# Performance work log

Hardware: AMD Instinct MI355X
Metric: run time of the kernel (lower is better)

Reference implementation:

```python
import jax, jax.numpy as jnp
import numpy as np

# physical params matching init_kwargs: (eta, gamma, Lambda, omega, n), dt
ETA, GAMMA, LAMBDA, OMEGA, NBAR = 0.8, 0.3, 0.5, 1.0, 2.0
DT = 1e-3


def _consts():
    a_diag = jnp.diag(jnp.full((2,), -0.5 * GAMMA, dtype=jnp.float32))
    d = jnp.diag(jnp.full((2,), GAMMA * (NBAR + 0.5) + LAMBDA, dtype=jnp.float32))
    c = jnp.diag(jnp.full((2,), np.float32(np.sqrt(4.0 * ETA * LAMBDA)), dtype=jnp.float32))
    sympl = jnp.array([[0.0, 1.0], [-1.0, 0.0]], dtype=jnp.float32)
    return a_diag, d, c, sympl


def setup_inputs() -> dict:
    key = jax.random.key(0)
    k1, k2 = jax.random.split(key)
    B, T = 8192, 2048
    dy = jax.random.normal(k1, (B, T, 2), dtype=jnp.float32) * 0.01  # measurement increments
    x0 = jnp.zeros((B, 2), dtype=jnp.float32)
    cov0 = jnp.zeros((B, 2, 2), dtype=jnp.float32)
    coeffs_A = jax.random.uniform(k2, (1, 1), dtype=jnp.float32, minval=-0.05, maxval=0.05)
    return {"dy": dy, "x0": x0, "cov0": cov0, "coeffs_A": coeffs_A}


def reference(dy, x0, cov0, coeffs_A):
    a_diag, D, C, sympl = _consts()
    # w == 1 branch: A = coeffs_A * symplectic + A_diag  ((1,1)*(2,2) broadcast)
    A = coeffs_A * sympl + a_diag
    Ct, Dt, At = C.T, D.T, A.T

    def step(carry, dy_t):
        sts, cov = carry  # [B,2], [B,2,2]
        out = jnp.einsum('ij,bj->bi', C, sts) * DT
        xicov = jnp.einsum('bij,jk->bik', cov, Ct) + Dt
        a_minus_xic = A - jnp.einsum('bij,jk->bik', xicov, C)
        x = sts + jnp.einsum('bij,bj->bi', a_minus_xic, sts) * DT \
                + jnp.einsum('bij,bj->bi', xicov, dy_t)
        cov_dt = (jnp.einsum('ij,bjk->bik', A, cov)
                  + jnp.einsum('bij,jk->bik', cov, At)
                  + D
                  - jnp.einsum('bij,bkj->bik', xicov, xicov))  # xicov @ xicov^T
        return (x, cov + cov_dt * DT), out

    _, outs = jax.lax.scan(step, (x0, cov0), jnp.swapaxes(dy, 0, 1))  # scan over T
    return jnp.swapaxes(outs, 0, 1)  # [B,T,2]
```

## Files before the change

### kernel.cpp

```cpp
#include <hip/hip_runtime.h>
#include <math.h>


typedef float nfloat4 __attribute__((ext_vector_type(4)));

template <int CTRL, int ROW_MASK>
__device__ __forceinline__ float dpp0(float x) {
    return __int_as_float(__builtin_amdgcn_update_dpp(
        0, __float_as_int(x), CTRL, ROW_MASK, 0xf, false));
}

__device__ __forceinline__ float wave_scan_add(float x) {
    x += dpp0<0x111, 0xf>(x);
    x += dpp0<0x112, 0xf>(x);
    x += dpp0<0x114, 0xf>(x);
    x += dpp0<0x118, 0xf>(x);
    x += dpp0<0x142, 0xa>(x);
    x += dpp0<0x143, 0xc>(x);
    return x;
}

__global__ __launch_bounds__(256) void setup_kernel(
    const float* __restrict__ cov0,
    const float* __restrict__ coeffs,
    float* __restrict__ utab,
    float* __restrict__ vtab)
{
    __shared__ float php[2048];
    __shared__ float phd[2048];
    __shared__ float phh[2048];
    __shared__ float3 Ee[32];
    __shared__ float Del[32];
    __shared__ double2 agg[4];

    const double cdD = sqrt(4.0 * 0.8 * 0.5);
    const double ddD = 0.3 * (2.0 + 0.5) + 0.5;
    const double adD = -0.5 * 0.3;
    const double aD  = -1e-3 * (cdD * cdD);
    const double bD  = 1.0 + 1e-3 * (2.0 * adD - 2.0 * cdD * ddD);
    const double cDc = 1e-3 * (ddD - ddD * ddD);

    const float cC   = (float)cdD;
    const float dcon = (float)ddD;
    const float ad   = (float)adD;
    const float A2   = (float)aD;
    const float B1   = (float)bD;
    const float C0   = (float)cDc;

    const double kap = 1e-3 * (double)coeffs[0];
    const double cdt = cdD * 1e-3;

    const int tid  = threadIdx.x;
    const int lane = tid & 63;
    const int wid  = tid >> 6;

    const double beta = bD - 1.0;
    const float pstar = (float)((-beta - sqrt(beta * beta - 4.0 * aD * cDc)) / (2.0 * aD));

    if (tid < 32) {
        float p   = (tid == 0) ? cov0[0] : pstar;
        float dch = 1.0f, hch = 0.0f;
        const int base = tid * 64;
        for (int i = 0; i < 64; ++i) {
            php[base + i] = p;
            phd[base + i] = dch;
            phh[base + i] = hch;
            float lam = fmaf(2.0f * A2, p, B1);
            hch = fmaf(lam, hch, A2 * dch * dch);
            dch = lam * dch;
            p   = fmaf(fmaf(A2, p, B1), p, C0);
        }
        Ee[tid] = make_float3(p, dch, hch);
    }
    __syncthreads();
    if (tid == 0) {
        float D = 0.0f;
        Del[0] = 0.0f;
        for (int c = 0; c < 31; ++c) {
            float3 e = Ee[c];
            float tn = e.x + D * fmaf(e.z, D, e.y);
            D = tn - pstar;
            Del[c + 1] = D;
        }
    }
    __syncthreads();

    const float Dl = Del[tid >> 3];
    float sv[8], mv[8];
    double Pr = 1.0, Pi = 0.0;
#pragma unroll
    for (int e = 0; e < 8; ++e) {
        int t = tid * 8 + e;
        float p = php[t] + Dl * fmaf(phh[t], Dl, phd[t]);
        float s = fmaf(cC, p, dcon);
        float m = fmaf(1e-3f, fmaf(-cC, s, ad), 1.0f);
        sv[e] = s; mv[e] = m;
        double nr = (double)m * Pr + kap * Pi;
        double ni = (double)m * Pi - kap * Pr;
        Pr = nr; Pi = ni;
    }

    double vr = Pr, vi = Pi;
#pragma unroll
    for (int delta = 1; delta < 64; delta <<= 1) {
        double ur = __shfl_up(vr, delta);
        double ui = __shfl_up(vi, delta);
        if (lane >= delta) {
            double nr = ur * vr - ui * vi;
            double ni = ur * vi + ui * vr;
            vr = nr; vi = ni;
        }
    }
    if (lane == 63) agg[wid] = make_double2(vr, vi);
    double exr = __shfl_up(vr, 1), exi = __shfl_up(vi, 1);
    if (lane == 0) { exr = 1.0; exi = 0.0; }
    __syncthreads();

    double br = 1.0, bi = 0.0;
    for (int w = 0; w < wid; ++w) {
        double2 a = agg[w];
        double nr = br * a.x - bi * a.y;
        double ni = br * a.y + bi * a.x;
        br = nr; bi = ni;
    }
    double Gr = br * exr - bi * exi;
    double Gi = br * exi + bi * exr;

    float uo[16], vo[16];
#pragma unroll
    for (int e = 0; e < 8; ++e) {
        vo[2 * e]     = (float)(cdt * Gr);
        vo[2 * e + 1] = (float)(cdt * Gi);
        double nr = (double)mv[e] * Gr + kap * Gi;
        double ni = (double)mv[e] * Gi - kap * Gr;
        Gr = nr; Gi = ni;
        double inv = 1.0 / (Gr * Gr + Gi * Gi);
        uo[2 * e]     = (float)( (double)sv[e] * Gr * inv);
        uo[2 * e + 1] = (float)(-(double)sv[e] * Gi * inv);
    }

    float4* up4 = (float4*)utab;
    float4* vp4 = (float4*)vtab;
#pragma unroll
    for (int j = 0; j < 4; ++j) {
        up4[4 * tid + j] = make_float4(uo[4*j], uo[4*j+1], uo[4*j+2], uo[4*j+3]);
        vp4[4 * tid + j] = make_float4(vo[4*j], vo[4*j+1], vo[4*j+2], vo[4*j+3]);
    }
}

__global__ __launch_bounds__(256, 8) void fused_kernel(
    const float* __restrict__ dy,
    const float* __restrict__ x0,
    const float* __restrict__ utab,
    const float* __restrict__ vtab,
    float* __restrict__ out,
    int T)
{
    __shared__ float2 aggs[4][4];

    const int tid  = threadIdx.x;
    const int lane = tid & 63;
    const int wid  = tid >> 6;
    const int b    = blockIdx.x;

    const float4* __restrict__ up4 = reinterpret_cast<const float4*>(utab);
    const float4* __restrict__ vp4 = reinterpret_cast<const float4*>(vtab);
    const float4* __restrict__ dyv =
        reinterpret_cast<const float4*>(dy + (size_t)b * T * 2);
    nfloat4* __restrict__ outv =
        reinterpret_cast<nfloat4*>(out + (size_t)b * T * 2);

    const float x0r = x0[2 * b];
    const float x0i = x0[2 * b + 1];

    float2 q[8], qq[4];
#pragma unroll
    for (int j = 0; j < 4; ++j) {
        float4 d = dyv[j * 256 + tid];
        float4 u = up4[j * 256 + tid];
        q[2*j].x   = fmaf(u.x, d.x, -(u.y * d.y));
        q[2*j].y   = fmaf(u.x, d.y,  (u.y * d.x));
        q[2*j+1].x = fmaf(u.z, d.z, -(u.w * d.w));
        q[2*j+1].y = fmaf(u.z, d.w,  (u.w * d.z));
        qq[j].x = q[2*j].x + q[2*j+1].x;
        qq[j].y = q[2*j].y + q[2*j+1].y;
    }

    float4 vt[4];
#pragma unroll
    for (int j = 0; j < 4; ++j) vt[j] = vp4[j * 256 + tid];

    float2 incl[4];
#pragma unroll
    for (int j = 0; j < 4; ++j) {
        incl[j].x = wave_scan_add(qq[j].x);
        incl[j].y = wave_scan_add(qq[j].y);
    }
    if (lane == 63) {
#pragma unroll
        for (int j = 0; j < 4; ++j) aggs[j][wid] = incl[j];
    }
    __syncthreads();

    float2 run = make_float2(x0r, x0i);
    float2 Sst[4];
#pragma unroll
    for (int j = 0; j < 4; ++j) {
        float2 wp  = make_float2(0.f, 0.f);
        float2 tot = make_float2(0.f, 0.f);
#pragma unroll
        for (int w = 0; w < 4; ++w) {
            float2 a = aggs[j][w];
            tot.x += a.x; tot.y += a.y;
            if (w < wid) { wp.x += a.x; wp.y += a.y; }
        }
        Sst[j].x = run.x + wp.x + (incl[j].x - qq[j].x);
        Sst[j].y = run.y + wp.y + (incl[j].y - qq[j].y);
        run.x += tot.x; run.y += tot.y;
    }

#pragma unroll
    for (int j = 0; j < 4; ++j) {
        float4 w = vt[j];
        float2 S = Sst[j];
        nfloat4 o;
        o.x = fmaf(w.x, S.x, -(w.y * S.y));
        o.y = fmaf(w.x, S.y,  (w.y * S.x));
        S.x += q[2*j].x; S.y += q[2*j].y;
        o.z = fmaf(w.z, S.x, -(w.w * S.y));
        o.w = fmaf(w.z, S.y,  (w.w * S.x));
        __builtin_nontemporal_store(o, &outv[j * 256 + tid]);
    }
}

extern "C" void kernel_launch(void* const* d_in, const int* in_sizes, int n_in,
                              void* d_out, int out_size, void* d_ws, size_t ws_size,
                              hipStream_t stream)
{
    const float* dy     = (const float*)d_in[0];
    const float* x0     = (const float*)d_in[1];
    const float* cov0   = (const float*)d_in[2];
    const float* coeffs = (const float*)d_in[3];
    float* out = (float*)d_out;

    const int B = in_sizes[1] / 2;
    const int T = in_sizes[0] / in_sizes[1];

    float* utab = (float*)d_ws;
    float* vtab = utab + 4096;

    setup_kernel<<<1, 256, 0, stream>>>(cov0, coeffs, utab, vtab);
    fused_kernel<<<B, 256, 0, stream>>>(dy, x0, utab, vtab, out, T);
}
```

Baseline: 49.46 us.

## Fuse setup table computation into main kernel, recomputing per block in LDS

Removes the separate single-block setup kernel and has every block recompute the gain/propagator tables directly into shared memory, with the per-chunk covariance recursion parallelized across threads. This eliminates a kernel launch, a serial single-block stage and the global round trip for the tables. In exchange each block performs redundant fp64 scans, serial loops and divisions, and uses 32KB of LDS, which may reduce occupancy and delay the streaming phase.

New measurement: 90.85 us. 83.7% more time.

```diff
diff --git a/kernel.cpp b/kernel.cpp
--- a/kernel.cpp
+++ b/kernel.cpp
@@ -20,18 +20,35 @@
     return x;
 }
 
-__global__ __launch_bounds__(256) void setup_kernel(
+__global__ __launch_bounds__(256) void fused_kernel(
+    const float* __restrict__ dy,
+    const float* __restrict__ x0,
     const float* __restrict__ cov0,
     const float* __restrict__ coeffs,
-    float* __restrict__ utab,
-    float* __restrict__ vtab)
+    float* __restrict__ out,
+    int T)
 {
-    __shared__ float php[2048];
-    __shared__ float phd[2048];
-    __shared__ float phh[2048];
+    __shared__ float4 uL[1024];
+    __shared__ float4 vL[1024];
     __shared__ float3 Ee[32];
-    __shared__ float Del[32];
-    __shared__ double2 agg[4];
+    __shared__ float  Del[32];
+    __shared__ double2 dagg[4];
+    __shared__ float2 aggs[4][4];
+
+    const int tid  = threadIdx.x;
+    const int lane = tid & 63;
+    const int wid  = tid >> 6;
+    const int b    = blockIdx.x;
+
+    const float4* __restrict__ dyv =
+        reinterpret_cast<const float4*>(dy + (size_t)b * T * 2);
+    nfloat4* __restrict__ outv =
+        reinterpret_cast<nfloat4*>(out + (size_t)b * T * 2);
+    float4 d4[4];
+#pragma unroll
+    for (int j = 0; j < 4; ++j) d4[j] = dyv[j * 256 + tid];
+    const float x0r = x0[2 * b];
+    const float x0i = x0[2 * b + 1];
 
     const double cdD = sqrt(4.0 * 0.8 * 0.5);
     const double ddD = 0.3 * (2.0 + 0.5) + 0.5;
@@ -39,61 +56,59 @@
     const double aD  = -1e-3 * (cdD * cdD);
     const double bD  = 1.0 + 1e-3 * (2.0 * adD - 2.0 * cdD * ddD);
     const double cDc = 1e-3 * (ddD - ddD * ddD);
-
     const float cC   = (float)cdD;
     const float dcon = (float)ddD;
     const float ad   = (float)adD;
     const float A2   = (float)aD;
     const float B1   = (float)bD;
     const float C0   = (float)cDc;
-
     const double kap = 1e-3 * (double)coeffs[0];
     const double cdt = cdD * 1e-3;
-
-    const int tid  = threadIdx.x;
-    const int lane = tid & 63;
-    const int wid  = tid >> 6;
-
     const double beta = bD - 1.0;
     const float pstar = (float)((-beta - sqrt(beta * beta - 4.0 * aD * cDc)) / (2.0 * aD));
 
-    if (tid < 32) {
-        float p   = (tid == 0) ? cov0[0] : pstar;
-        float dch = 1.0f, hch = 0.0f;
-        const int base = tid * 64;
-        for (int i = 0; i < 64; ++i) {
-            php[base + i] = p;
-            phd[base + i] = dch;
-            phh[base + i] = hch;
-            float lam = fmaf(2.0f * A2, p, B1);
-            hch = fmaf(lam, hch, A2 * dch * dch);
-            dch = lam * dch;
-            p   = fmaf(fmaf(A2, p, B1), p, C0);
-        }
-        Ee[tid] = make_float3(p, dch, hch);
-    }
-    __syncthreads();
+    const int c  = tid >> 3;
+    const int qp = tid & 7;
+    float p   = (c == 0) ? cov0[0] : pstar;
+    float dch = 1.0f, hch = 0.0f;
+    for (int i = 0; i < 8 * qp; ++i) {
+        float lam = fmaf(2.0f * A2, p, B1);
+        hch = fmaf(lam, hch, A2 * dch * dch);
+        dch = lam * dch;
+        p   = fmaf(fmaf(A2, p, B1), p, C0);
+    }
+    float kp[8], kd[8], kh[8];
+#pragma unroll
+    for (int e = 0; e < 8; ++e) {
+        kp[e] = p; kd[e] = dch; kh[e] = hch;
+        float lam = fmaf(2.0f * A2, p, B1);
+        hch = fmaf(lam, hch, A2 * dch * dch);
+        dch = lam * dch;
+        p   = fmaf(fmaf(A2, p, B1), p, C0);
+    }
+    if (qp == 7) Ee[c] = make_float3(p, dch, hch);
+    __syncthreads();
+
     if (tid == 0) {
         float D = 0.0f;
         Del[0] = 0.0f;
-        for (int c = 0; c < 31; ++c) {
-            float3 e = Ee[c];
+        for (int cc = 0; cc < 31; ++cc) {
+            float3 e = Ee[cc];
             float tn = e.x + D * fmaf(e.z, D, e.y);
             D = tn - pstar;
-            Del[c + 1] = D;
+            Del[cc + 1] = D;
         }
     }
     __syncthreads();
-
-    const float Dl = Del[tid >> 3];
+    const float Dl = Del[c];
+
     float sv[8], mv[8];
     double Pr = 1.0, Pi = 0.0;
 #pragma unroll
     for (int e = 0; e < 8; ++e) {
-        int t = tid * 8 + e;
-        float p = php[t] + Dl * fmaf(phh[t], Dl, phd[t]);
-        float s = fmaf(cC, p, dcon);
-        float m = fmaf(1e-3f, fmaf(-cC, s, ad), 1.0f);
+        float pc = kp[e] + Dl * fmaf(kh[e], Dl, kd[e]);
+        float s  = fmaf(cC, pc, dcon);
+        float m  = fmaf(1e-3f, fmaf(-cC, s, ad), 1.0f);
         sv[e] = s; mv[e] = m;
         double nr = (double)m * Pr + kap * Pi;
         double ni = (double)m * Pi - kap * Pr;
@@ -111,14 +126,14 @@
             vr = nr; vi = ni;
         }
     }
-    if (lane == 63) agg[wid] = make_double2(vr, vi);
+    if (lane == 63) dagg[wid] = make_double2(vr, vi);
     double exr = __shfl_up(vr, 1), exi = __shfl_up(vi, 1);
     if (lane == 0) { exr = 1.0; exi = 0.0; }
     __syncthreads();
 
     double br = 1.0, bi = 0.0;
     for (int w = 0; w < wid; ++w) {
-        double2 a = agg[w];
+        double2 a = dagg[w];
         double nr = br * a.x - bi * a.y;
         double ni = br * a.y + bi * a.x;
         br = nr; bi = ni;
@@ -138,46 +153,18 @@
         uo[2 * e]     = (float)( (double)sv[e] * Gr * inv);
         uo[2 * e + 1] = (float)(-(double)sv[e] * Gi * inv);
     }
-
-    float4* up4 = (float4*)utab;
-    float4* vp4 = (float4*)vtab;
-#pragma unroll
-    for (int j = 0; j < 4; ++j) {
-        up4[4 * tid + j] = make_float4(uo[4*j], uo[4*j+1], uo[4*j+2], uo[4*j+3]);
-        vp4[4 * tid + j] = make_float4(vo[4*j], vo[4*j+1], vo[4*j+2], vo[4*j+3]);
-    }
-}
-
-__global__ __launch_bounds__(256, 8) void fused_kernel(
-    const float* __restrict__ dy,
-    const float* __restrict__ x0,
-    const float* __restrict__ utab,
-    const float* __restrict__ vtab,
-    float* __restrict__ out,
-    int T)
-{
-    __shared__ float2 aggs[4][4];
-
-    const int tid  = threadIdx.x;
-    const int lane = tid & 63;
-    const int wid  = tid >> 6;
-    const int b    = blockIdx.x;
-
-    const float4* __restrict__ up4 = reinterpret_cast<const float4*>(utab);
-    const float4* __restrict__ vp4 = reinterpret_cast<const float4*>(vtab);
-    const float4* __restrict__ dyv =
-        reinterpret_cast<const float4*>(dy + (size_t)b * T * 2);
-    nfloat4* __restrict__ outv =
-        reinterpret_cast<nfloat4*>(out + (size_t)b * T * 2);
-
-    const float x0r = x0[2 * b];
-    const float x0i = x0[2 * b + 1];
+#pragma unroll
+    for (int j = 0; j < 4; ++j) {
+        uL[4 * tid + j] = make_float4(uo[4*j], uo[4*j+1], uo[4*j+2], uo[4*j+3]);
+        vL[4 * tid + j] = make_float4(vo[4*j], vo[4*j+1], vo[4*j+2], vo[4*j+3]);
+    }
+    __syncthreads();
 
     float2 q[8], qq[4];
 #pragma unroll
     for (int j = 0; j < 4; ++j) {
-        float4 d = dyv[j * 256 + tid];
-        float4 u = up4[j * 256 + tid];
+        float4 d = d4[j];
+        float4 u = uL[j * 256 + tid];
         q[2*j].x   = fmaf(u.x, d.x, -(u.y * d.y));
         q[2*j].y   = fmaf(u.x, d.y,  (u.y * d.x));
         q[2*j+1].x = fmaf(u.z, d.z, -(u.w * d.w));
@@ -185,10 +172,6 @@
         qq[j].x = q[2*j].x + q[2*j+1].x;
         qq[j].y = q[2*j].y + q[2*j+1].y;
     }
-
-    float4 vt[4];
-#pragma unroll
-    for (int j = 0; j < 4; ++j) vt[j] = vp4[j * 256 + tid];
 
     float2 incl[4];
 #pragma unroll
@@ -221,7 +204,7 @@
 
 #pragma unroll
     for (int j = 0; j < 4; ++j) {
-        float4 w = vt[j];
+        float4 w = vL[j * 256 + tid];
         float2 S = Sst[j];
         nfloat4 o;
         o.x = fmaf(w.x, S.x, -(w.y * S.y));
@@ -246,9 +229,5 @@
     const int B = in_sizes[1] / 2;
     const int T = in_sizes[0] / in_sizes[1];
 
-    float* utab = (float*)d_ws;
-    float* vtab = utab + 4096;
-
-    setup_kernel<<<1, 256, 0, stream>>>(cov0, coeffs, utab, vtab);
-    fused_kernel<<<B, 256, 0, stream>>>(dy, x0, utab, vtab, out, T);
-}
+    fused_kernel<<<B, 256, 0, stream>>>(dy, x0, cov0, coeffs, out, T);
+}
```
